# Kernel optimization log

Hardware: AMD Instinct MI355X
Metric: run time of the kernel (lower is better)

Reference implementation:

```python
import jax, jax.numpy as jnp
import numpy as np

B, T, D = 4, 2048, 1024
H, KVH = 16, 4          # query heads, kv heads
HD = D // H             # head_dim = 64
R = 32                  # partial rope dims
ROPE_BASE = 10000.0
EPS = 1e-6


def rmsnorm(x, scale):
    # per-head RMSNorm over last dim, computed in fp32 like the torch code
    xf = x.astype(jnp.float32)
    norm = jax.lax.rsqrt(jnp.mean(xf * xf, axis=-1, keepdims=True) + EPS)
    return (xf * norm).astype(x.dtype) * scale


def apply_rope(x, cos, sin):
    # x: (B,T,H,HD); rotate first R dims, pass the rest through
    x_r, x_p = x[..., :R], x[..., R:]
    half = R // 2
    x1, x2 = x_r[..., :half], x_r[..., half:]
    rotated = jnp.concatenate([x1 * cos - x2 * sin, x1 * sin + x2 * cos], axis=-1)
    return jnp.concatenate([rotated, x_p], axis=-1)


def setup_inputs() -> dict:
    key = jax.random.key(0)
    ks = jax.random.split(key, 8)
    x = jax.random.normal(ks[0], (B, T, D), dtype=jnp.float32)
    # RoPE tables exactly as RotaryEmbedding.get_cos_sin
    inv_freq = 1.0 / (ROPE_BASE ** (jnp.arange(0, R, 2, dtype=jnp.float32) / R))
    t = jnp.arange(T, dtype=jnp.float32)
    freqs = jnp.outer(t, inv_freq)                      # (T, R/2)
    cos = jnp.cos(freqs)[None, :, None, :]              # (1,T,1,R/2)
    sin = jnp.sin(freqs)[None, :, None, :]
    s = 1.0 / np.sqrt(D)
    Wq = jax.random.normal(ks[1], (D, D), dtype=jnp.float32) * s
    Wk = jax.random.normal(ks[2], (KVH * HD, D), dtype=jnp.float32) * s
    Wv = jax.random.normal(ks[3], (KVH * HD, D), dtype=jnp.float32) * s
    Wo = jax.random.normal(ks[4], (D, D), dtype=jnp.float32) * s
    q_scale = jnp.ones((HD,), dtype=jnp.float32)
    k_scale = jnp.ones((HD,), dtype=jnp.float32)
    return {"x": x, "cos": cos, "sin": sin, "Wq": Wq, "Wk": Wk, "Wv": Wv,
            "Wo": Wo, "q_scale": q_scale, "k_scale": k_scale}


def reference(x, cos, sin, Wq, Wk, Wv, Wo, q_scale, k_scale):
    b, t, d = x.shape
    q = jnp.einsum('btd,ed->bte', x, Wq).reshape(b, t, H, HD)
    k = jnp.einsum('btd,ed->bte', x, Wk).reshape(b, t, KVH, HD)
    v = jnp.einsum('btd,ed->bte', x, Wv).reshape(b, t, KVH, HD)
    q = apply_rope(rmsnorm(q, q_scale), cos, sin)
    k = apply_rope(rmsnorm(k, k_scale), cos, sin)
    groups = H // KVH
    k = jnp.repeat(k, groups, axis=2)   # (b,t,H,HD), matches repeat_interleave dim=2
    v = jnp.repeat(v, groups, axis=2)
    q = q.transpose(0, 2, 1, 3)         # (b,H,t,HD)
    k = k.transpose(0, 2, 1, 3)
    v = v.transpose(0, 2, 1, 3)
    scores = jnp.einsum('bhqd,bhkd->bhqk', q, k) / np.sqrt(HD)
    causal = jnp.tril(jnp.ones((t, t), dtype=bool))
    scores = jnp.where(causal, scores, -jnp.inf)
    attn = jax.nn.softmax(scores, axis=-1)
    y = jnp.einsum('bhqk,bhkd->bhqd', attn, v)
    y = y.transpose(0, 2, 1, 3).reshape(b, t, d)
    return jnp.einsum('btd,ed->bte', y, Wo)
```

## Files before the change

kernel.cpp:

```cpp
#include <hip/hip_runtime.h>
#include <hip/hip_bf16.h>
#include <stdint.h>

typedef __attribute__((ext_vector_type(8)))  __bf16 bf16x8;
typedef __attribute__((ext_vector_type(4)))  float  f32x4;
typedef __attribute__((ext_vector_type(16))) float  f32x16;
typedef __hip_bfloat16 bf16_t;

#define T_SEQ 2048
#define D_MODEL 1024
#define N_HEADS 16
#define N_KV 4
#define HD 64
#define LDQKV 1536
#define KDIM 1024

__device__ inline void cvt16(const float4* __restrict__ g, int4* __restrict__ s) {
  float4 v0 = g[0], v1 = g[1], v2 = g[2], v3 = g[3];
  union { int4 i[2]; __hip_bfloat162 h[8]; } u;
  u.h[0] = __float22bfloat162_rn(make_float2(v0.x, v0.y));
  u.h[1] = __float22bfloat162_rn(make_float2(v0.z, v0.w));
  u.h[2] = __float22bfloat162_rn(make_float2(v1.x, v1.y));
  u.h[3] = __float22bfloat162_rn(make_float2(v1.z, v1.w));
  u.h[4] = __float22bfloat162_rn(make_float2(v2.x, v2.y));
  u.h[5] = __float22bfloat162_rn(make_float2(v2.z, v2.w));
  u.h[6] = __float22bfloat162_rn(make_float2(v3.x, v3.y));
  u.h[7] = __float22bfloat162_rn(make_float2(v3.z, v3.w));
  s[0] = u.i[0]; s[1] = u.i[1];
}

__device__ inline void storeC(bf16_t* p, float v) { *p = __float2bfloat16(v); }
__device__ inline void storeC(float* p, float v) { *p = v; }

__device__ inline void plswap(unsigned& a, unsigned& b) {
  asm volatile("v_permlane32_swap_b32 %0, %1" : "+v"(a), "+v"(b));
}

__device__ inline float fexp2(float x) {
  float r; asm("v_exp_f32 %0, %1" : "=v"(r) : "v"(x)); return r;
}
__device__ inline unsigned cvtpk(float lo, float hi) {
  unsigned r; asm("v_cvt_pk_bf16_f32 %0, %1, %2" : "=v"(r) : "v"(lo), "v"(hi));
  return r;
}

__device__ inline void gll16(const bf16_t* g, bf16_t* l) {
  __builtin_amdgcn_global_load_lds(
      (const __attribute__((address_space(1))) void*)g,
      (__attribute__((address_space(3))) void*)l, 16, 0, 0);
}

__global__ __launch_bounds__(256) void all_cvt(
    const float* __restrict__ x,
    const float* __restrict__ Wq, const float* __restrict__ Wk,
    const float* __restrict__ Wv, const float* __restrict__ Wo,
    bf16_t* __restrict__ xb, bf16_t* __restrict__ wqkvb,
    bf16_t* __restrict__ wob) {
  const int i = blockIdx.x * 256 + threadIdx.x;
  const float* s; bf16_t* d; int off;
  if (i < 524288)      { s = x;  d = xb;                   off = i; }
  else if (i < 589824) { s = Wq; d = wqkvb;                off = i - 524288; }
  else if (i < 606208) { s = Wk; d = wqkvb + 1024 * 1024;  off = i - 589824; }
  else if (i < 622592) { s = Wv; d = wqkvb + 1280 * 1024;  off = i - 606208; }
  else                 { s = Wo; d = wob;                  off = i - 622592; }
  cvt16((const float4*)s + off * 4, (int4*)d + off * 2);
}

template <int MODE, int NX, typename CT>
__global__ __launch_bounds__(256) void gemm_bb(
    const bf16_t* __restrict__ A, const bf16_t* __restrict__ W,
    CT* __restrict__ C, const int ldC,
    const float* __restrict__ cosb, const float* __restrict__ sinb,
    const float* __restrict__ qs, const float* __restrict__ ks,
    bf16_t* __restrict__ v_t)
{
  __shared__ bf16_t Smem[32768];
  const int tid = threadIdx.x;
  const int lane = tid & 63;
  const int wv = tid >> 6;
  const int wr = wv >> 1, wc = wv & 1;
  const int id  = (int)blockIdx.x;
  const int xcd = id & 7;
  const int seq = id >> 3;
  const int mp  = (seq / NX) * 8 + xcd;
  const int nt  = seq - (seq / NX) * NX;
  const int m0 = mp * 128;
  const int n0 = nt * 128;

  const int srow = lane >> 2;
  const int scol = (lane & 3) * 8;
  const bf16_t* gA = A + (size_t)(m0 + 32 * wv + srow) * KDIM + scol;
  const bf16_t* gB = W + (size_t)(n0 + 32 * wv + srow) * KDIM + scol;
  const int lOff = wv * 1024;

  f32x4 acc[4][4];
#pragma unroll
  for (int m = 0; m < 4; ++m)
#pragma unroll
    for (int n = 0; n < 4; ++n)
      acc[m][n] = {0.f, 0.f, 0.f, 0.f};

  const int fr = lane & 15;
  const int fq = lane >> 4;

#define STAGE_GEMM(bufb, kk) {                                        \
    bf16_t* _bs = Smem + (bufb) * 16384 + lOff;                       \
    gll16(gA + (kk), _bs);                                            \
    gll16(gA + 16 * KDIM + (kk), _bs + 512);                          \
    gll16(gA + (kk) + 32, _bs + 4096);                                \
    gll16(gA + 16 * KDIM + (kk) + 32, _bs + 4608);                    \
    gll16(gB + (kk), _bs + 8192);                                     \
    gll16(gB + 16 * KDIM + (kk), _bs + 8704);                         \
    gll16(gB + (kk) + 32, _bs + 12288);                               \
    gll16(gB + 16 * KDIM + (kk) + 32, _bs + 12800);                   \
  }

  STAGE_GEMM(0, 0);
  __syncthreads();

  int buf = 0;
  for (int r = 0; r < 16; ++r) {
    if (r + 1 < 16) STAGE_GEMM(buf ^ 1, (r + 1) * 64);
    const bf16_t* base = Smem + buf * 16384;
#pragma unroll
    for (int half = 0; half < 2; ++half) {
      const bf16_t* As = base + half * 4096;
      const bf16_t* Bs = base + 8192 + half * 4096;
      bf16x8 af[4], bfv[4];
#pragma unroll
      for (int m = 0; m < 4; ++m)
        af[m] = *(const bf16x8*)(&As[(wr * 64 + m * 16 + fr) * 32 + fq * 8]);
#pragma unroll
      for (int n = 0; n < 4; ++n)
        bfv[n] = *(const bf16x8*)(&Bs[(wc * 64 + n * 16 + fr) * 32 + fq * 8]);
#pragma unroll
      for (int m = 0; m < 4; ++m)
#pragma unroll
        for (int n = 0; n < 4; ++n)
          acc[m][n] = __builtin_amdgcn_mfma_f32_16x16x32_bf16(af[m], bfv[n],
                                                              acc[m][n], 0, 0, 0);
    }
    __syncthreads();
    buf ^= 1;
  }
#undef STAGE_GEMM

  if (MODE == 0 || n0 < 1280) {
    if (MODE == 1) {
      const float* stab = (n0 < 1024) ? qs : ks;
      float sc0 = stab[fr], sc1 = stab[16 + fr], sc2 = stab[32 + fr], sc3 = stab[48 + fr];
#pragma unroll
      for (int m = 0; m < 4; ++m)
#pragma unroll
        for (int r = 0; r < 4; ++r) {
          const int row = m0 + wr * 64 + m * 16 + fq * 4 + r;
          const int t = row & (T_SEQ - 1);
          float ss = acc[m][0][r] * acc[m][0][r] + acc[m][1][r] * acc[m][1][r]
                   + acc[m][2][r] * acc[m][2][r] + acc[m][3][r] * acc[m][3][r];
          ss += __shfl_xor(ss, 1);
          ss += __shfl_xor(ss, 2);
          ss += __shfl_xor(ss, 4);
          ss += __shfl_xor(ss, 8);
          const float nrm = rsqrtf(ss * (1.f / 64.f) + 1e-6f);
          const float v0 = acc[m][0][r] * nrm * sc0;
          const float v1 = acc[m][1][r] * nrm * sc1;
          const float v2 = acc[m][2][r] * nrm * sc2;
          const float v3 = acc[m][3][r] * nrm * sc3;
          const float c = cosb[t * 16 + fr];
          const float s = sinb[t * 16 + fr];
          union { unsigned u; bf16_t hh[2]; } pa, pb;
          pa.u = cvtpk(v0 * c - v1 * s, v0 * s + v1 * c);
          pb.u = cvtpk(v2, v3);
          bf16_t* p = (bf16_t*)C + (size_t)row * ldC + n0 + wc * 64 + fr;
          p[0]  = pa.hh[0];
          p[16] = pa.hh[1];
          p[32] = pb.hh[0];
          p[48] = pb.hh[1];
        }
    } else {
#pragma unroll
      for (int m = 0; m < 4; ++m)
#pragma unroll
        for (int n = 0; n < 4; ++n)
#pragma unroll
          for (int r = 0; r < 4; ++r) {
            const int row = wr * 64 + m * 16 + fq * 4 + r;
            const int col = wc * 64 + n * 16 + fr;
            storeC(&C[(size_t)(m0 + row) * ldC + n0 + col], acc[m][n][r]);
          }
    }
  } else {
    const int b4 = (m0 >> 11) * 4;
    const int t0base = m0 & (T_SEQ - 1);
    const int vcol = tid & 127;
    const int vc = n0 - 1280 + vcol;
    const int g = b4 + (vc >> 6);
    const int d = vc & 63;
#pragma unroll
    for (int half = 0; half < 2; ++half) {
      if (wr == half) {
#pragma unroll
        for (int m = 0; m < 4; ++m)
#pragma unroll
          for (int n = 0; n < 4; ++n)
#pragma unroll
            for (int r2 = 0; r2 < 4; r2 += 2) {
              union { unsigned u; bf16_t hh[2]; } pk2;
              pk2.u = cvtpk(acc[m][n][r2], acc[m][n][r2 + 1]);
              const int tl0 = m * 16 + fq * 4 + r2;
              const int col = wc * 64 + n * 16 + fr;
              const int sw = ((tl0 >> 2) & 7) << 4;
              Smem[tl0 * 128 + (col ^ sw)]       = pk2.hh[0];
              Smem[(tl0 + 1) * 128 + (col ^ sw)] = pk2.hh[1];
            }
      }
      __syncthreads();
      bf16_t* dst0 = v_t + ((size_t)(g * HD + d)) * T_SEQ + t0base + half * 64;
#pragma unroll
      for (int ci = 0; ci < 2; ++ci) {
        const int cu = (tid >> 7) + ci * 2;
        union { int4 q[2]; bf16_t hh[16]; } ld;
#pragma unroll
        for (int t = 0; t < 16; ++t) {
          const int tt = cu * 16 + t;
          ld.hh[t] = Smem[tt * 128 + (vcol ^ (((tt >> 2) & 7) << 4))];
        }
        *(int4*)(dst0 + cu * 16)     = ld.q[0];
        *(int4*)(dst0 + cu * 16 + 8) = ld.q[1];
      }
      __syncthreads();
    }
  }
}

__global__ __launch_bounds__(512) void attn(
    const bf16_t* __restrict__ qkv, const bf16_t* __restrict__ v_t,
    bf16_t* __restrict__ y)
{
  __shared__ int4 lds[2048];
  const int tid  = threadIdx.x;
  const int lane = tid & 63;
  const int w    = tid >> 6;
  const int spair= w >> 1;
  const int h    = w & 1;
  const int ql   = lane & 31;
  const int hi   = lane >> 5;
  const int id   = (int)blockIdx.x;
  const int low3 = id & 7;
  const int rest = id >> 3;
  const int gsel = rest & 1;
  const int hh   = (rest >> 1) & 3;
  const int sbi  = rest >> 3;
  const int sb   = ((sbi >> 2) & 1) ? (sbi + 4 - ((sbi >> 3) << 4)) : (15 - sbi);
  const int g16  = low3 + 8 * gsel;
  const int b    = g16 >> 2, kvh = g16 & 3;
  const int hd   = kvh * 4 + hh;
  const int s    = 4 * sb + spair;
  const int q_glob = s * 32 + ql;
  const int nt   = s + 1;
  const int nR   = 2 * sb + 2;
  const float SCALE_LOG2 = 0.125f * 1.44269504089f;

  const int sid = tid & 255;
  const int u   = tid >> 8;
  const int kr = sid >> 3, kslot = sid & 7;
  const int vd = sid >> 2, vslot = sid & 3;
  const bf16_t* gK = qkv + (size_t)(b * T_SEQ + kr + u * 32) * LDQKV + 1024 + kvh * HD + kslot * 8;
  const bf16_t* gV = v_t + (size_t)((b * N_KV + kvh) * HD + vd) * T_SEQ + vslot * 8 + u * 32;
  const int wKidx = u * 256 + kr * 8 + (kslot ^ (kr & 7));
  const int wVidx = 512 + u * 256 + vd * 4 + (vslot ^ ((vd >> 1) & 3));

  int kridx[4];
#pragma unroll
  for (int c = 0; c < 4; ++c)
    kridx[c] = ql * 8 + ((2 * c + hi) ^ (ql & 7));
  const int vsw = (ql >> 1) & 3;
  const int v0idx = 512 + ql * 4 + (hi ^ vsw);
  const int v1idx = 512 + ql * 4 + ((2 + hi) ^ vsw);
  const int v2idx = 512 + (ql + 32) * 4 + (hi ^ vsw);
  const int v3idx = 512 + (ql + 32) * 4 + ((2 + hi) ^ vsw);

  union ob { unsigned uu[4]; bf16x8 v; } onesf;
#pragma unroll
  for (int i = 0; i < 4; ++i) onesf.uu[i] = 0x3F803F80u;

  f32x16 zro;
#pragma unroll
  for (int i = 0; i < 16; ++i) zro[i] = 0.f;

  float* lf = (float*)lds;

  const bf16_t* Qrow = qkv + (size_t)(b * T_SEQ + q_glob) * LDQKV + hd * HD + hi * 8;
  bf16x8 qfrag[4];
#pragma unroll
  for (int c = 0; c < 4; ++c) {
    bf16x8 raw = *(const bf16x8*)(Qrow + c * 16);
    bf16x8 sc;
#pragma unroll
    for (int j = 0; j < 8; ++j)
      sc[j] = (__bf16)((float)raw[j] * SCALE_LOG2);
    qfrag[c] = sc;
  }

  f32x16 acc0, acc1, accL;
#pragma unroll
  for (int i = 0; i < 16; ++i) { acc0[i] = 0.f; acc1[i] = 0.f; accL[i] = 0.f; }
  float m_run = -1e30f;

  {
    int4 kA = *(const int4*)gK;
    int4 vA = *(const int4*)gV;
    lds[wKidx] = kA;
    lds[wVidx] = vA;
  }
  __syncthreads();

  int buf = 0;
  for (int r = 0; r < nR; ++r) {
    int4 kA, vA;
    const bool more = (r + 1 < nR);
    if (more) {
      kA = *(const int4*)(gK + (size_t)(r + 1) * 64 * LDQKV);
      vA = *(const int4*)(gV + (r + 1) * 64);
    }

    const int t = 2 * r + h;
    if (t < nt) {
      const int k0 = t << 5;
      const bool masked = (t == nt - 1);
      const int base = buf * 1024 + h * 256;

      bf16x8 kf0 = *(const bf16x8*)&lds[base + kridx[0]];
      bf16x8 kf1 = *(const bf16x8*)&lds[base + kridx[1]];
      bf16x8 kf2 = *(const bf16x8*)&lds[base + kridx[2]];
      bf16x8 kf3 = *(const bf16x8*)&lds[base + kridx[3]];

      __builtin_amdgcn_s_setprio(1);
      f32x16 st = __builtin_amdgcn_mfma_f32_32x32x16_bf16(kf0, qfrag[0], zro, 0, 0, 0);
      st = __builtin_amdgcn_mfma_f32_32x32x16_bf16(kf1, qfrag[1], st, 0, 0, 0);
      st = __builtin_amdgcn_mfma_f32_32x32x16_bf16(kf2, qfrag[2], st, 0, 0, 0);
      st = __builtin_amdgcn_mfma_f32_32x32x16_bf16(kf3, qfrag[3], st, 0, 0, 0);
      __builtin_amdgcn_s_setprio(0);

      if (masked) {
#pragma unroll
        for (int rr = 0; rr < 16; ++rr) {
          const int kg = k0 + (rr & 3) + 8 * (rr >> 2) + 4 * hi;
          if (kg > q_glob) st[rr] = -1e30f;
        }
      }
      float m01 = fmaxf(fmaxf(st[0], st[1]), st[2]);
      float m02 = fmaxf(fmaxf(st[3], st[4]), st[5]);
      float m03 = fmaxf(fmaxf(st[6], st[7]), st[8]);
      float m04 = fmaxf(fmaxf(st[9], st[10]), st[11]);
      float m05 = fmaxf(fmaxf(st[12], st[13]), st[14]);
      float m06 = fmaxf(fmaxf(m01, m02), m03);
      float m07 = fmaxf(fmaxf(m04, m05), st[15]);
      const float bmax = fmaxf(m06, m07);
      if (__any(bmax > m_run + 8.f)) {
        const float rmax = fmaxf(bmax, __shfl_xor(bmax, 32));
        const float mnew = fmaxf(m_run, rmax);
        const float corr = fexp2(m_run - mnew);
#pragma unroll
        for (int i = 0; i < 16; ++i) { acc0[i] *= corr; acc1[i] *= corr; }
        accL[0] *= corr;
        m_run = mnew;
      }
      float pp[16];
#pragma unroll
      for (int rr = 0; rr < 16; ++rr) pp[rr] = fexp2(st[rr] - m_run);

      unsigned wp[8];
#pragma unroll
      for (int i = 0; i < 8; ++i) wp[i] = cvtpk(pp[2 * i], pp[2 * i + 1]);
      plswap(wp[0], wp[2]); plswap(wp[1], wp[3]);
      plswap(wp[4], wp[6]); plswap(wp[5], wp[7]);
      union fu { unsigned uu2[4]; bf16x8 v; };
      fu f1, f2;
      f1.uu2[0] = wp[0]; f1.uu2[1] = wp[1]; f1.uu2[2] = wp[2]; f1.uu2[3] = wp[3];
      f2.uu2[0] = wp[4]; f2.uu2[1] = wp[5]; f2.uu2[2] = wp[6]; f2.uu2[3] = wp[7];

      bf16x8 vf0 = *(const bf16x8*)&lds[base + v0idx];
      bf16x8 vf1 = *(const bf16x8*)&lds[base + v1idx];
      bf16x8 vf2 = *(const bf16x8*)&lds[base + v2idx];
      bf16x8 vf3 = *(const bf16x8*)&lds[base + v3idx];

      __builtin_amdgcn_s_setprio(1);
      acc0 = __builtin_amdgcn_mfma_f32_32x32x16_bf16(vf0, f1.v, acc0, 0, 0, 0);
      acc0 = __builtin_amdgcn_mfma_f32_32x32x16_bf16(vf1, f2.v, acc0, 0, 0, 0);
      acc1 = __builtin_amdgcn_mfma_f32_32x32x16_bf16(vf2, f1.v, acc1, 0, 0, 0);
      acc1 = __builtin_amdgcn_mfma_f32_32x32x16_bf16(vf3, f2.v, acc1, 0, 0, 0);
      accL = __builtin_amdgcn_mfma_f32_32x32x16_bf16(onesf.v, f1.v, accL, 0, 0, 0);
      accL = __builtin_amdgcn_mfma_f32_32x32x16_bf16(onesf.v, f2.v, accL, 0, 0, 0);
      __builtin_amdgcn_s_setprio(0);
    }

    if (more) {
      const int nb = (buf ^ 1) * 1024;
      lds[nb + wKidx] = kA;
      lds[nb + wVidx] = vA;
    }
    __syncthreads();
    buf ^= 1;
  }

  float cA = 1.f, cB = 0.f, l_mrg = 0.f;
  if (h == 1) {
    const int fb = spair * 1216 + lane * 19;
#pragma unroll
    for (int i = 0; i < 16; ++i) lf[fb + i] = acc0[i];
    lf[fb + 16] = m_run;
    lf[fb + 17] = accL[0];
  }
  __syncthreads();
  if (h == 0) {
    const int fb = spair * 1216 + lane * 19;
    const float mB = lf[fb + 16], lB = lf[fb + 17];
    const float mM = fmaxf(m_run, mB);
    cA = fexp2(m_run - mM);
    cB = fexp2(mB - mM);
    l_mrg = accL[0] * cA + lB * cB;
#pragma unroll
    for (int i = 0; i < 16; ++i) acc0[i] = acc0[i] * cA + lf[fb + i] * cB;
  }
  __syncthreads();
  if (h == 1) {
    const int fb2 = spair * 1088 + lane * 17;
#pragma unroll
    for (int i = 0; i < 16; ++i) lf[fb2 + i] = acc1[i];
  }
  __syncthreads();
  if (h == 0) {
    const int fb2 = spair * 1088 + lane * 17;
#pragma unroll
    for (int i = 0; i < 16; ++i) acc1[i] = acc1[i] * cA + lf[fb2 + i] * cB;
    const float inv = 1.f / l_mrg;
    bf16_t* yrow = y + (size_t)(b * T_SEQ + q_glob) * D_MODEL + hd * HD;
#pragma unroll
    for (int gg = 0; gg < 4; ++gg) {
      uint2 o0, o1;
      o0.x = cvtpk(acc0[4 * gg + 0] * inv, acc0[4 * gg + 1] * inv);
      o0.y = cvtpk(acc0[4 * gg + 2] * inv, acc0[4 * gg + 3] * inv);
      o1.x = cvtpk(acc1[4 * gg + 0] * inv, acc1[4 * gg + 1] * inv);
      o1.y = cvtpk(acc1[4 * gg + 2] * inv, acc1[4 * gg + 3] * inv);
      *(uint2*)(yrow + 8 * gg + 4 * hi)      = o0;
      *(uint2*)(yrow + 32 + 8 * gg + 4 * hi) = o1;
    }
  }
}

extern "C" void kernel_launch(void* const* d_in, const int* in_sizes, int n_in,
                              void* d_out, int out_size, void* d_ws,
                              size_t ws_size, hipStream_t stream) {
  const float* x    = (const float*)d_in[0];
  const float* cosb = (const float*)d_in[1];
  const float* sinb = (const float*)d_in[2];
  const float* Wq   = (const float*)d_in[3];
  const float* Wk   = (const float*)d_in[4];
  const float* Wv   = (const float*)d_in[5];
  const float* Wo   = (const float*)d_in[6];
  const float* qs   = (const float*)d_in[7];
  const float* ks   = (const float*)d_in[8];
  float* out = (float*)d_out;

  char* ws = (char*)d_ws;
  bf16_t* qkv   = (bf16_t*)ws;
  bf16_t* v_t   = (bf16_t*)(ws + 25165824);
  bf16_t* y     = (bf16_t*)(ws + 29360128);
  bf16_t* xb    = y;
  bf16_t* wqkvb = (bf16_t*)(ws + 46137344);
  bf16_t* wob   = (bf16_t*)(ws + 49283072);

  all_cvt<<<dim3(2688), 256, 0, stream>>>(x, Wq, Wk, Wv, Wo, xb, wqkvb, wob);

  gemm_bb<1, 12, bf16_t><<<dim3(768), 256, 0, stream>>>(
      xb, wqkvb, qkv, LDQKV, cosb, sinb, qs, ks, v_t);
  attn<<<dim3(1024), 512, 0, stream>>>(qkv, v_t, y);
  gemm_bb<0, 8, float><<<dim3(512), 256, 0, stream>>>(
      y, wob, out, D_MODEL, nullptr, nullptr, nullptr, nullptr, nullptr);
}
```

Measured before the change: 135.7 us.

## Halve attention block to 256 threads with 64-row query tiles and reverse scheduling

The attention kernel now uses 256-thread blocks that each cover two 32-row query strips, instead of 512-thread blocks covering four, and the grid doubles to 2048 blocks. Each thread now loads two K and two V 16-byte chunks per 64-key round. The number of rounds per block now follows the smaller tile, which is meant to cut idle waves on the causal diagonal and give finer load balancing. The old permuted super-block order is replaced by a simple longest-first reverse order. In exchange, each K/V tile is shared by fewer query rows, so global and LDS traffic per query rises.

```diff
diff --git a/kernel.cpp b/kernel.cpp
--- a/kernel.cpp
+++ b/kernel.cpp
@@ -233,7 +233,7 @@
   }
 }
 
-__global__ __launch_bounds__(512) void attn(
+__global__ __launch_bounds__(256) void attn(
     const bf16_t* __restrict__ qkv, const bf16_t* __restrict__ v_t,
     bf16_t* __restrict__ y)
 {
@@ -250,25 +250,26 @@
   const int rest = id >> 3;
   const int gsel = rest & 1;
   const int hh   = (rest >> 1) & 3;
-  const int sbi  = rest >> 3;
-  const int sb   = ((sbi >> 2) & 1) ? (sbi + 4 - ((sbi >> 3) << 4)) : (15 - sbi);
+  const int sp   = 31 - (rest >> 3);
   const int g16  = low3 + 8 * gsel;
   const int b    = g16 >> 2, kvh = g16 & 3;
   const int hd   = kvh * 4 + hh;
-  const int s    = 4 * sb + spair;
+  const int s    = 2 * sp + spair;
   const int q_glob = s * 32 + ql;
   const int nt   = s + 1;
-  const int nR   = 2 * sb + 2;
+  const int nR   = sp + 1;
   const float SCALE_LOG2 = 0.125f * 1.44269504089f;
 
-  const int sid = tid & 255;
-  const int u   = tid >> 8;
-  const int kr = sid >> 3, kslot = sid & 7;
-  const int vd = sid >> 2, vslot = sid & 3;
-  const bf16_t* gK = qkv + (size_t)(b * T_SEQ + kr + u * 32) * LDQKV + 1024 + kvh * HD + kslot * 8;
-  const bf16_t* gV = v_t + (size_t)((b * N_KV + kvh) * HD + vd) * T_SEQ + vslot * 8 + u * 32;
-  const int wKidx = u * 256 + kr * 8 + (kslot ^ (kr & 7));
-  const int wVidx = 512 + u * 256 + vd * 4 + (vslot ^ ((vd >> 1) & 3));
+  const int kr = tid >> 3, kslot = tid & 7;
+  const int vd = tid >> 2, vslot = tid & 3;
+  const bf16_t* gK0 = qkv + (size_t)(b * T_SEQ + kr) * LDQKV + 1024 + kvh * HD + kslot * 8;
+  const bf16_t* gK1 = gK0 + (size_t)32 * LDQKV;
+  const bf16_t* gV0 = v_t + (size_t)((b * N_KV + kvh) * HD + vd) * T_SEQ + vslot * 8;
+  const bf16_t* gV1 = gV0 + 32;
+  const int wK0 = kr * 8 + (kslot ^ (kr & 7));
+  const int wK1 = 256 + wK0;
+  const int wV0 = 512 + vd * 4 + (vslot ^ ((vd >> 1) & 3));
+  const int wV1 = 256 + wV0;
 
   int kridx[4];
 #pragma unroll
@@ -308,20 +309,26 @@
   float m_run = -1e30f;
 
   {
-    int4 kA = *(const int4*)gK;
-    int4 vA = *(const int4*)gV;
-    lds[wKidx] = kA;
-    lds[wVidx] = vA;
+    int4 a0 = *(const int4*)gK0;
+    int4 a1 = *(const int4*)gK1;
+    int4 a2 = *(const int4*)gV0;
+    int4 a3 = *(const int4*)gV1;
+    lds[wK0] = a0; lds[wK1] = a1;
+    lds[wV0] = a2; lds[wV1] = a3;
   }
   __syncthreads();
 
   int buf = 0;
   for (int r = 0; r < nR; ++r) {
-    int4 kA, vA;
+    int4 a0, a1, a2, a3;
     const bool more = (r + 1 < nR);
     if (more) {
-      kA = *(const int4*)(gK + (size_t)(r + 1) * 64 * LDQKV);
-      vA = *(const int4*)(gV + (r + 1) * 64);
+      const size_t kAdv = (size_t)(r + 1) * 64 * LDQKV;
+      const int vAdv = (r + 1) * 64;
+      a0 = *(const int4*)(gK0 + kAdv);
+      a1 = *(const int4*)(gK1 + kAdv);
+      a2 = *(const int4*)(gV0 + vAdv);
+      a3 = *(const int4*)(gV1 + vAdv);
     }
 
     const int t = 2 * r + h;
@@ -397,8 +404,8 @@
 
     if (more) {
       const int nb = (buf ^ 1) * 1024;
-      lds[nb + wKidx] = kA;
-      lds[nb + wVidx] = vA;
+      lds[nb + wK0] = a0; lds[nb + wK1] = a1;
+      lds[nb + wV0] = a2; lds[nb + wV1] = a3;
     }
     __syncthreads();
     buf ^= 1;
@@ -475,7 +482,7 @@
 
   gemm_bb<1, 12, bf16_t><<<dim3(768), 256, 0, stream>>>(
       xb, wqkvb, qkv, LDQKV, cosb, sinb, qs, ks, v_t);
-  attn<<<dim3(1024), 512, 0, stream>>>(qkv, v_t, y);
+  attn<<<dim3(2048), 256, 0, stream>>>(qkv, v_t, y);
   gemm_bb<0, 8, float><<<dim3(512), 256, 0, stream>>>(
       y, wob, out, D_MODEL, nullptr, nullptr, nullptr, nullptr, nullptr);
 }
```

After: 154.0 us. 13.5% more time.
